# Optimization experiments

Measured on AMD Instinct MI355X. Metric: run time of the kernel, lower is better.

## Reference

```python
import jax, jax.numpy as jnp
import numpy as np

N = 50000
E = 800000
HID = 128
EIN = 2 * HID + 1  # h[row] ++ h[col] ++ edge_attr
NC = 3             # n_coords
DIM = 3            # spatial dim
NORM_FACTOR = 100.0
LN_EPS = 1e-5


def layernorm(x, g, b):
    m = jnp.mean(x, axis=-1, keepdims=True)
    v = jnp.mean(jnp.square(x - m), axis=-1, keepdims=True)
    return (x - m) * jax.lax.rsqrt(v + LN_EPS) * g + b


def setup_inputs() -> dict:
    key = jax.random.key(0)
    ks = jax.random.split(key, 12)
    h = jax.random.normal(ks[0], (N, HID), dtype=jnp.float32)
    coord = jax.random.normal(ks[1], (N, NC, DIM), dtype=jnp.float32)
    coord_diff = jax.random.normal(ks[2], (E, NC, DIM), dtype=jnp.float32)
    edge_attr = jax.random.normal(ks[3], (E, 1), dtype=jnp.float32)
    edge_mask = jnp.ones((E, 1), dtype=jnp.float32)
    node_mask = jnp.ones((N, 1, 1), dtype=jnp.float32)
    row = jax.random.randint(ks[4], (E,), 0, N, dtype=jnp.int32)
    col = jax.random.randint(ks[5], (E,), 0, N, dtype=jnp.int32)
    # MLP params (stored [in, out])
    def xavier(k, fi, fo, gain=1.0):
        lim = gain * np.sqrt(6.0 / (fi + fo))
        return jax.random.uniform(k, (fi, fo), dtype=jnp.float32, minval=-lim, maxval=lim)
    W1 = xavier(ks[6], EIN, HID)
    b1 = jnp.zeros((HID,), jnp.float32)
    g1 = jnp.ones((HID,), jnp.float32)
    be1 = jnp.zeros((HID,), jnp.float32)
    W2 = xavier(ks[7], HID, HID)
    b2 = jnp.zeros((HID,), jnp.float32)
    g2 = jnp.ones((HID,), jnp.float32)
    be2 = jnp.zeros((HID,), jnp.float32)
    W3 = xavier(ks[8], HID, NC * NC, gain=0.01)  # final layer, no bias
    return dict(h=h, coord=coord, coord_diff=coord_diff, edge_attr=edge_attr,
                edge_mask=edge_mask, node_mask=node_mask, row=row, col=col,
                W1=W1, b1=b1, g1=g1, be1=be1, W2=W2, b2=b2, g2=g2, be2=be2, W3=W3)


def reference(h, coord, coord_diff, edge_attr, edge_mask, node_mask, row, col,
              W1, b1, g1, be1, W2, b2, g2, be2, W3):
    # gather node feats into edge features: [E, 2*HID + 1]
    x = jnp.concatenate([h[row], h[col], edge_attr], axis=1)
    x = jax.nn.silu(layernorm(x @ W1 + b1, g1, be1))
    x = jax.nn.silu(layernorm(x @ W2 + b2, g2, be2))
    phi = (x @ W3).reshape(-1, NC, NC)               # [E, NC, NC]
    trans = jnp.einsum('ejk,ejl->elk', coord_diff, phi)  # [E, NC, DIM]
    trans = trans * edge_mask[:, None]               # [E,1,1] broadcast
    agg = jax.ops.segment_sum(trans, row, num_segments=coord.shape[0]) / NORM_FACTOR
    return (coord + agg) * node_mask
```

## Files before the change

### kernel.cpp

```cpp
#include <hip/hip_runtime.h>
#include <hip/hip_bf16.h>

#define NN 50000
#define EE 800000

typedef __attribute__((ext_vector_type(8))) short short8;
typedef __attribute__((ext_vector_type(4))) short short4v;
typedef __attribute__((ext_vector_type(4))) float f32x4;

__device__ __forceinline__ float bf2f(ushort u) {
  union { unsigned u; float f; } v; v.u = ((unsigned)u) << 16; return v.f;
}
__device__ __forceinline__ ushort f2bf(float f) {
  union { float f; unsigned u; } v; v.f = f;
  unsigned r = v.u + 0x7FFFu + ((v.u >> 16) & 1u);
  return (ushort)(r >> 16);
}

__global__ void prep_h_kernel(const float* __restrict__ h, ushort* __restrict__ hb) {
  int i = blockIdx.x * 256 + threadIdx.x;
  const float4* p = (const float4*)h;
  float4 a = p[2*i], b = p[2*i+1];
  short8 o;
  o[0]=f2bf(a.x); o[1]=f2bf(a.y); o[2]=f2bf(a.z); o[3]=f2bf(a.w);
  o[4]=f2bf(b.x); o[5]=f2bf(b.y); o[6]=f2bf(b.z); o[7]=f2bf(b.w);
  *(short8*)(hb + 8*i) = o;
}

__global__ void prep_w_kernel(const float* __restrict__ W1, const float* __restrict__ W2,
                              const float* __restrict__ W3,
                              ushort* __restrict__ W1t, ushort* __restrict__ W2t,
                              ushort* __restrict__ W3t) {
  int i = blockIdx.x * 256 + threadIdx.x;
  if (i < 32768) {
    int n = i >> 8, k = i & 255;
    W1t[i] = f2bf(W1[k*128 + n]);
  } else if (i < 49152) {
    int j = i - 32768, n = j >> 7, k = j & 127;
    W2t[j] = f2bf(W2[k*128 + n]);
  } else if (i < 51200) {
    int j = i - 49152, n = j >> 7, k = j & 127;
    W3t[j] = (n < 9) ? f2bf(W3[k*9 + n]) : (ushort)0;
  }
}

__device__ __forceinline__ void ln_silu(const ushort* smT, ushort* smX,
                                        float* smRedS, float* smRedQ,
                                        const float* __restrict__ g,
                                        const float* __restrict__ be,
                                        int lane, int w) {
  int e = lane, n0 = w * 32;
  float s = 0.f, q = 0.f;
  #pragma unroll
  for (int i = 0; i < 32; ++i) {
    float f = bf2f(smT[(n0 + i)*72 + e]);
    s += f; q += f*f;
  }
  smRedS[w*64 + e] = s; smRedQ[w*64 + e] = q;
  __syncthreads();
  s = smRedS[e] + smRedS[64+e] + smRedS[128+e] + smRedS[192+e];
  q = smRedQ[e] + smRedQ[64+e] + smRedQ[128+e] + smRedQ[192+e];
  float m  = s * (1.f/128.f);
  float rs = rsqrtf(q * (1.f/128.f) - m*m + 1e-5f);
  #pragma unroll
  for (int c = 0; c < 4; ++c) {
    short8 o;
    #pragma unroll
    for (int j = 0; j < 8; ++j) {
      int i = c*8 + j;
      float f = bf2f(smT[(n0 + i)*72 + e]);
      float v = (f - m) * rs * g[n0 + i] + be[n0 + i];
      v = v * (1.f / (1.f + __expf(-v)));
      o[j] = f2bf(v);
    }
    int bo = (e*256 + (n0 + c*8)*2) ^ ((e & 7) << 4);
    *(short8*)((char*)smX + bo) = o;
  }
}

template<bool USE_HB>
__global__ __launch_bounds__(256, 2)
void edge_kernel(const float* __restrict__ h, const ushort* __restrict__ hb,
                 const ushort* __restrict__ W1t, const ushort* __restrict__ W2t,
                 const ushort* __restrict__ W3t,
                 const float* __restrict__ W1,
                 const float* __restrict__ b1, const float* __restrict__ g1, const float* __restrict__ be1,
                 const float* __restrict__ b2, const float* __restrict__ g2, const float* __restrict__ be2,
                 const float* __restrict__ edge_attr, const float* __restrict__ edge_mask,
                 const float* __restrict__ coord_diff,
                 const int* __restrict__ row, const int* __restrict__ col,
                 float* __restrict__ agg) {
  __shared__ __align__(16) ushort smA[64*256];
  __shared__ __align__(16) ushort smT[128*72];
  __shared__ __align__(16) ushort smX[64*128];
  __shared__ float smCd[64*9];
  __shared__ float smPhi[64*12];
  __shared__ float smRedS[256];
  __shared__ float smRedQ[256];
  __shared__ float smEA[64];
  __shared__ float smEM[64];
  __shared__ int   smRow[64];

  const int tid  = threadIdx.x;
  const int lane = tid & 63;
  const int w    = tid >> 6;
  const int l15  = lane & 15;
  const int lh   = lane >> 4;
  const int wm   = w >> 1;
  const int wn   = w & 1;
  const int e0   = blockIdx.x * 64;

  {
    int e = tid >> 2, p = tid & 3;
    int re = row[e0 + e], ce = col[e0 + e];
    if (p == 0) { smEA[e] = edge_attr[e0+e]; smEM[e] = edge_mask[e0+e]; smRow[e] = re; }
    if (USE_HB) {
      const ushort* s = hb + (size_t)((p & 2) ? ce : re) * 128 + (p & 1) * 64;
      #pragma unroll
      for (int c = 0; c < 8; ++c) {
        short8 v = *(const short8*)(s + c*8);
        int bo = (e*512 + (p*8 + c)*16) ^ ((e & 7) << 4);
        *(short8*)((char*)smA + bo) = v;
      }
    } else {
      const float* s = h + (size_t)((p & 2) ? ce : re) * 128 + (p & 1) * 64;
      #pragma unroll
      for (int c = 0; c < 8; ++c) {
        float4 a = *(const float4*)(s + c*8);
        float4 b = *(const float4*)(s + c*8 + 4);
        short8 v;
        v[0]=f2bf(a.x); v[1]=f2bf(a.y); v[2]=f2bf(a.z); v[3]=f2bf(a.w);
        v[4]=f2bf(b.x); v[5]=f2bf(b.y); v[6]=f2bf(b.z); v[7]=f2bf(b.w);
        int bo = (e*512 + (p*8 + c)*16) ^ ((e & 7) << 4);
        *(short8*)((char*)smA + bo) = v;
      }
    }
  }
  if (tid < 144)
    *(float4*)(smCd + tid*4) = *(const float4*)(coord_diff + (size_t)e0*9 + tid*4);
  __syncthreads();

  f32x4 acc[2][4] = {};
  {
    const ushort* Wp[4];
    #pragma unroll
    for (int nf = 0; nf < 4; ++nf)
      Wp[nf] = W1t + (size_t)(wn*64 + nf*16 + l15) * 256 + lh*8;
    #pragma unroll
    for (int k0 = 0; k0 < 8; ++k0) {
      short8 b[4];
      #pragma unroll
      for (int nf = 0; nf < 4; ++nf) b[nf] = *(const short8*)(Wp[nf] + k0*32);
      #pragma unroll
      for (int mi = 0; mi < 2; ++mi) {
        int r = wm*32 + mi*16 + l15;
        int bo = (r*512 + k0*64 + lh*16) ^ ((r & 7) << 4);
        short8 a = *(const short8*)((char*)smA + bo);
        #pragma unroll
        for (int nf = 0; nf < 4; ++nf)
          acc[mi][nf] = __builtin_amdgcn_mfma_f32_16x16x32_bf16(a, b[nf], acc[mi][nf], 0, 0, 0);
      }
    }
  }
  {
    const float* w1last = W1 + 256*128;
    #pragma unroll
    for (int nf = 0; nf < 4; ++nf) {
      int n = wn*64 + nf*16 + l15;
      float bb = b1[n], wl = w1last[n];
      #pragma unroll
      for (int mi = 0; mi < 2; ++mi) {
        int r0 = wm*32 + mi*16 + lh*4;
        short4v o;
        #pragma unroll
        for (int j = 0; j < 4; ++j)
          o[j] = f2bf(acc[mi][nf][j] + bb + smEA[r0 + j] * wl);
        *(short4v*)(smT + n*72 + r0) = o;
      }
    }
  }
  __syncthreads();
  ln_silu(smT, smX, smRedS, smRedQ, g1, be1, lane, w);
  __syncthreads();

  f32x4 acc2[2][4] = {};
  {
    const ushort* Wp[4];
    #pragma unroll
    for (int nf = 0; nf < 4; ++nf)
      Wp[nf] = W2t + (size_t)(wn*64 + nf*16 + l15) * 128 + lh*8;
    #pragma unroll
    for (int k0 = 0; k0 < 4; ++k0) {
      short8 b[4];
      #pragma unroll
      for (int nf = 0; nf < 4; ++nf) b[nf] = *(const short8*)(Wp[nf] + k0*32);
      #pragma unroll
      for (int mi = 0; mi < 2; ++mi) {
        int r = wm*32 + mi*16 + l15;
        int bo = (r*256 + k0*64 + lh*16) ^ ((r & 7) << 4);
        short8 a = *(const short8*)((char*)smX + bo);
        #pragma unroll
        for (int nf = 0; nf < 4; ++nf)
          acc2[mi][nf] = __builtin_amdgcn_mfma_f32_16x16x32_bf16(a, b[nf], acc2[mi][nf], 0, 0, 0);
      }
    }
  }
  {
    #pragma unroll
    for (int nf = 0; nf < 4; ++nf) {
      int n = wn*64 + nf*16 + l15;
      float bb = b2[n];
      #pragma unroll
      for (int mi = 0; mi < 2; ++mi) {
        int r0 = wm*32 + mi*16 + lh*4;
        short4v o;
        #pragma unroll
        for (int j = 0; j < 4; ++j) o[j] = f2bf(acc2[mi][nf][j] + bb);
        *(short4v*)(smT + n*72 + r0) = o;
      }
    }
  }
  __syncthreads();
  ln_silu(smT, smX, smRedS, smRedQ, g2, be2, lane, w);
  __syncthreads();

  {
    f32x4 acc3 = {};
    const ushort* Wp = W3t + (size_t)l15*128 + lh*8;
    #pragma unroll
    for (int k0 = 0; k0 < 4; ++k0) {
      short8 b = *(const short8*)(Wp + k0*32);
      int r = w*16 + l15;
      int bo = (r*256 + k0*64 + lh*16) ^ ((r & 7) << 4);
      short8 a = *(const short8*)((char*)smX + bo);
      acc3 = __builtin_amdgcn_mfma_f32_16x16x32_bf16(a, b, acc3, 0, 0, 0);
    }
    if (l15 < 9) {
      #pragma unroll
      for (int j = 0; j < 4; ++j)
        smPhi[(w*16 + lh*4 + j)*12 + l15] = acc3[j];
    }
  }
  __syncthreads();

  {
    int e = tid >> 2, q = tid & 3;
    int re = smRow[e];
    float em = smEM[e];
    const float* cd = smCd + e*9;
    const float* ph = smPhi + e*12;
    for (int idx = q; idx < 9; idx += 4) {
      int l2 = idx / 3, k = idx - l2*3;
      float t = cd[k]*ph[l2] + cd[3+k]*ph[3+l2] + cd[6+k]*ph[6+l2];
      unsafeAtomicAdd(&agg[(size_t)re*9 + idx], t * em);
    }
  }
}

__global__ void finalize_kernel(const float* __restrict__ coord, const float* __restrict__ node_mask,
                                const float* __restrict__ agg, float* __restrict__ out) {
  int i = blockIdx.x * 256 + threadIdx.x;
  if (i < NN*9) {
    int n = i / 9;
    out[i] = (coord[i] + agg[i] * 0.01f) * node_mask[n];
  }
}

extern "C" void kernel_launch(void* const* d_in, const int* in_sizes, int n_in,
                              void* d_out, int out_size, void* d_ws, size_t ws_size,
                              hipStream_t stream) {
  const float* h          = (const float*)d_in[0];
  const float* coord      = (const float*)d_in[1];
  const float* coord_diff = (const float*)d_in[2];
  const float* edge_attr  = (const float*)d_in[3];
  const float* edge_mask  = (const float*)d_in[4];
  const float* node_mask  = (const float*)d_in[5];
  const int*   rowi       = (const int*)d_in[6];
  const int*   coli       = (const int*)d_in[7];
  const float* W1  = (const float*)d_in[8];
  const float* b1  = (const float*)d_in[9];
  const float* g1  = (const float*)d_in[10];
  const float* be1 = (const float*)d_in[11];
  const float* W2  = (const float*)d_in[12];
  const float* b2  = (const float*)d_in[13];
  const float* g2  = (const float*)d_in[14];
  const float* be2 = (const float*)d_in[15];
  const float* W3  = (const float*)d_in[16];

  char* ws = (char*)d_ws;
  float*  agg = (float*)ws;
  ushort* W1t = (ushort*)(ws + 1800064);
  ushort* W2t = (ushort*)(ws + 1865600);
  ushort* W3t = (ushort*)(ws + 1898368);
  ushort* hb  = (ushort*)(ws + 1902464);
  bool use_hb = ws_size >= (size_t)1902464 + 12800000;

  hipMemsetAsync(agg, 0, (size_t)NN*9*sizeof(float), stream);
  prep_w_kernel<<<200, 256, 0, stream>>>(W1, W2, W3, W1t, W2t, W3t);
  if (use_hb) {
    prep_h_kernel<<<NN*128/(8*256), 256, 0, stream>>>(h, hb);
    edge_kernel<true><<<EE/64, 256, 0, stream>>>(h, hb, W1t, W2t, W3t, W1,
        b1, g1, be1, b2, g2, be2, edge_attr, edge_mask, coord_diff, rowi, coli, agg);
  } else {
    edge_kernel<false><<<EE/64, 256, 0, stream>>>(h, hb, W1t, W2t, W3t, W1,
        b1, g1, be1, b2, g2, be2, edge_attr, edge_mask, coord_diff, rowi, coli, agg);
  }
  finalize_kernel<<<(NN*9 + 255)/256, 256, 0, stream>>>(coord, node_mask, agg, (float*)d_out);
}
```

Before: 601.9 us.

## Alias shared buffers, do LayerNorm in place, merge prep launches, raise occupancy

The MFMA outputs are now written straight into the swizzled row-major activation buffer. LayerNorm+SiLU then runs in place, with each thread caching its 32 values in registers, so the transposed staging buffer is gone. The gather buffer and activation buffer share one shared-memory region, which cuts LDS per block from about 75KB to 35KB, and launch bounds are raised to allow 4 blocks per CU. The weight/h bf16 conversion kernels and the agg memset are merged into one prep launch, and SiLU uses a hardware reciprocal. In exchange there are extra barriers, scalar 2-byte LDS stores that may bank-conflict, and higher register pressure under the tighter launch bound.

```diff
diff --git a/kernel.cpp b/kernel.cpp
--- a/kernel.cpp
+++ b/kernel.cpp
@@ -5,7 +5,6 @@
 #define EE 800000
 
 typedef __attribute__((ext_vector_type(8))) short short8;
-typedef __attribute__((ext_vector_type(4))) short short4v;
 typedef __attribute__((ext_vector_type(4))) float f32x4;
 
 __device__ __forceinline__ float bf2f(ushort u) {
@@ -17,46 +16,54 @@
   return (ushort)(r >> 16);
 }
 
-__global__ void prep_h_kernel(const float* __restrict__ h, ushort* __restrict__ hb) {
-  int i = blockIdx.x * 256 + threadIdx.x;
-  const float4* p = (const float4*)h;
-  float4 a = p[2*i], b = p[2*i+1];
-  short8 o;
-  o[0]=f2bf(a.x); o[1]=f2bf(a.y); o[2]=f2bf(a.z); o[3]=f2bf(a.w);
-  o[4]=f2bf(b.x); o[5]=f2bf(b.y); o[6]=f2bf(b.z); o[7]=f2bf(b.w);
-  *(short8*)(hb + 8*i) = o;
-}
-
-__global__ void prep_w_kernel(const float* __restrict__ W1, const float* __restrict__ W2,
-                              const float* __restrict__ W3,
-                              ushort* __restrict__ W1t, ushort* __restrict__ W2t,
-                              ushort* __restrict__ W3t) {
-  int i = blockIdx.x * 256 + threadIdx.x;
-  if (i < 32768) {
-    int n = i >> 8, k = i & 255;
-    W1t[i] = f2bf(W1[k*128 + n]);
-  } else if (i < 49152) {
-    int j = i - 32768, n = j >> 7, k = j & 127;
-    W2t[j] = f2bf(W2[k*128 + n]);
-  } else if (i < 51200) {
-    int j = i - 49152, n = j >> 7, k = j & 127;
-    W3t[j] = (n < 9) ? f2bf(W3[k*9 + n]) : (ushort)0;
-  }
-}
-
-__device__ __forceinline__ void ln_silu(const ushort* smT, ushort* smX,
-                                        float* smRedS, float* smRedQ,
-                                        const float* __restrict__ g,
-                                        const float* __restrict__ be,
-                                        int lane, int w) {
-  int e = lane, n0 = w * 32;
-  float s = 0.f, q = 0.f;
+__global__ void prep_kernel(const float* __restrict__ h, ushort* __restrict__ hb,
+                            const float* __restrict__ W1, const float* __restrict__ W2,
+                            const float* __restrict__ W3,
+                            ushort* __restrict__ W1t, ushort* __restrict__ W2t,
+                            ushort* __restrict__ W3t, float* __restrict__ agg) {
+  int b = blockIdx.x, tid = threadIdx.x;
+  if (b < 3125) {
+    int i = b * 256 + tid;
+    const float4* p = (const float4*)h;
+    float4 a = p[2*i], c = p[2*i+1];
+    short8 o;
+    o[0]=f2bf(a.x); o[1]=f2bf(a.y); o[2]=f2bf(a.z); o[3]=f2bf(a.w);
+    o[4]=f2bf(c.x); o[5]=f2bf(c.y); o[6]=f2bf(c.z); o[7]=f2bf(c.w);
+    *(short8*)(hb + 8*i) = o;
+  } else if (b < 3325) {
+    int i = (b - 3125) * 256 + tid;
+    if (i < 32768) {
+      int n = i >> 8, k = i & 255;
+      W1t[i] = f2bf(W1[k*128 + n]);
+    } else if (i < 49152) {
+      int j = i - 32768, n = j >> 7, k = j & 127;
+      W2t[j] = f2bf(W2[k*128 + n]);
+    } else if (i < 51200) {
+      int j = i - 49152, n = j >> 7, k = j & 127;
+      W3t[j] = (n < 9) ? f2bf(W3[k*9 + n]) : (ushort)0;
+    }
+  } else {
+    int i = (b - 3325) * 256 + tid;
+    if (i < NN*9) agg[i] = 0.f;
+  }
+}
+
+__device__ __forceinline__ void ln_silu_inplace(ushort* smX, float* smRedS, float* smRedQ,
+                                                const float* __restrict__ g,
+                                                const float* __restrict__ be, int tid) {
+  int e = tid & 63, w4 = tid >> 6, n0 = w4 * 32;
+  float v[32]; float s = 0.f, q = 0.f;
+  int bo[4];
   #pragma unroll
-  for (int i = 0; i < 32; ++i) {
-    float f = bf2f(smT[(n0 + i)*72 + e]);
-    s += f; q += f*f;
-  }
-  smRedS[w*64 + e] = s; smRedQ[w*64 + e] = q;
+  for (int c = 0; c < 4; ++c) {
+    bo[c] = (e*256 + (n0 + c*8)*2) ^ ((e & 7) << 4);
+    short8 x = *(const short8*)((char*)smX + bo[c]);
+    #pragma unroll
+    for (int j = 0; j < 8; ++j) {
+      float f = bf2f((ushort)x[j]); v[c*8+j] = f; s += f; q += f*f;
+    }
+  }
+  smRedS[w4*64 + e] = s; smRedQ[w4*64 + e] = q;
   __syncthreads();
   s = smRedS[e] + smRedS[64+e] + smRedS[128+e] + smRedS[192+e];
   q = smRedQ[e] + smRedQ[64+e] + smRedQ[128+e] + smRedQ[192+e];
@@ -67,19 +74,17 @@
     short8 o;
     #pragma unroll
     for (int j = 0; j < 8; ++j) {
-      int i = c*8 + j;
-      float f = bf2f(smT[(n0 + i)*72 + e]);
-      float v = (f - m) * rs * g[n0 + i] + be[n0 + i];
-      v = v * (1.f / (1.f + __expf(-v)));
-      o[j] = f2bf(v);
-    }
-    int bo = (e*256 + (n0 + c*8)*2) ^ ((e & 7) << 4);
-    *(short8*)((char*)smX + bo) = o;
-  }
+      float val = (v[c*8+j] - m) * rs * g[n0 + c*8 + j] + be[n0 + c*8 + j];
+      val = val * __builtin_amdgcn_rcpf(1.f + __expf(-val));
+      o[j] = f2bf(val);
+    }
+    *(short8*)((char*)smX + bo[c]) = o;
+  }
+  __syncthreads();
 }
 
 template<bool USE_HB>
-__global__ __launch_bounds__(256, 2)
+__global__ __launch_bounds__(256, 4)
 void edge_kernel(const float* __restrict__ h, const ushort* __restrict__ hb,
                  const ushort* __restrict__ W1t, const ushort* __restrict__ W2t,
                  const ushort* __restrict__ W3t,
@@ -90,16 +95,16 @@
                  const float* __restrict__ coord_diff,
                  const int* __restrict__ row, const int* __restrict__ col,
                  float* __restrict__ agg) {
-  __shared__ __align__(16) ushort smA[64*256];
-  __shared__ __align__(16) ushort smT[128*72];
-  __shared__ __align__(16) ushort smX[64*128];
-  __shared__ float smCd[64*9];
-  __shared__ float smPhi[64*12];
-  __shared__ float smRedS[256];
-  __shared__ float smRedQ[256];
-  __shared__ float smEA[64];
-  __shared__ float smEM[64];
-  __shared__ int   smRow[64];
+  __shared__ __align__(16) char smem[35840];
+  ushort* smA   = (ushort*)smem;
+  ushort* smX   = (ushort*)smem;
+  float*  smRedS = (float*)(smem + 16384);
+  float*  smRedQ = (float*)(smem + 17408);
+  float*  smPhi  = (float*)(smem + 18432);
+  float*  smCd   = (float*)(smem + 32768);
+  float*  smEA   = (float*)(smem + 35072);
+  float*  smEM   = (float*)(smem + 35328);
+  int*    smRow  = (int*)  (smem + 35584);
 
   const int tid  = threadIdx.x;
   const int lane = tid & 63;
@@ -127,10 +132,10 @@
       #pragma unroll
       for (int c = 0; c < 8; ++c) {
         float4 a = *(const float4*)(s + c*8);
-        float4 b = *(const float4*)(s + c*8 + 4);
+        float4 bq = *(const float4*)(s + c*8 + 4);
         short8 v;
         v[0]=f2bf(a.x); v[1]=f2bf(a.y); v[2]=f2bf(a.z); v[3]=f2bf(a.w);
-        v[4]=f2bf(b.x); v[5]=f2bf(b.y); v[6]=f2bf(b.z); v[7]=f2bf(b.w);
+        v[4]=f2bf(bq.x); v[5]=f2bf(bq.y); v[6]=f2bf(bq.z); v[7]=f2bf(bq.w);
         int bo = (e*512 + (p*8 + c)*16) ^ ((e & 7) << 4);
         *(short8*)((char*)smA + bo) = v;
       }
@@ -162,26 +167,36 @@
       }
     }
   }
+  __syncthreads();
+
   {
     const float* w1last = W1 + 256*128;
+    float bbv[4], wlv[4];
     #pragma unroll
     for (int nf = 0; nf < 4; ++nf) {
       int n = wn*64 + nf*16 + l15;
-      float bb = b1[n], wl = w1last[n];
-      #pragma unroll
-      for (int mi = 0; mi < 2; ++mi) {
-        int r0 = wm*32 + mi*16 + lh*4;
-        short4v o;
+      bbv[nf] = b1[n]; wlv[nf] = w1last[n];
+    }
+    #pragma unroll
+    for (int mi = 0; mi < 2; ++mi) {
+      int r0 = wm*32 + mi*16 + lh*4;
+      float ea[4];
+      #pragma unroll
+      for (int j = 0; j < 4; ++j) ea[j] = smEA[r0 + j];
+      #pragma unroll
+      for (int nf = 0; nf < 4; ++nf) {
+        int n = wn*64 + nf*16 + l15;
         #pragma unroll
-        for (int j = 0; j < 4; ++j)
-          o[j] = f2bf(acc[mi][nf][j] + bb + smEA[r0 + j] * wl);
-        *(short4v*)(smT + n*72 + r0) = o;
-      }
-    }
-  }
-  __syncthreads();
-  ln_silu(smT, smX, smRedS, smRedQ, g1, be1, lane, w);
-  __syncthreads();
+        for (int j = 0; j < 4; ++j) {
+          int r = r0 + j;
+          float val = acc[mi][nf][j] + bbv[nf] + ea[j] * wlv[nf];
+          *(ushort*)((char*)smX + ((r*256 + n*2) ^ ((r & 7) << 4))) = f2bf(val);
+        }
+      }
+    }
+  }
+  __syncthreads();
+  ln_silu_inplace(smX, smRedS, smRedQ, g1, be1, tid);
 
   f32x4 acc2[2][4] = {};
   {
@@ -205,24 +220,29 @@
       }
     }
   }
-  {
-    #pragma unroll
-    for (int nf = 0; nf < 4; ++nf) {
-      int n = wn*64 + nf*16 + l15;
-      float bb = b2[n];
-      #pragma unroll
-      for (int mi = 0; mi < 2; ++mi) {
-        int r0 = wm*32 + mi*16 + lh*4;
-        short4v o;
+  __syncthreads();
+
+  {
+    float bbv[4];
+    #pragma unroll
+    for (int nf = 0; nf < 4; ++nf) bbv[nf] = b2[wn*64 + nf*16 + l15];
+    #pragma unroll
+    for (int mi = 0; mi < 2; ++mi) {
+      int r0 = wm*32 + mi*16 + lh*4;
+      #pragma unroll
+      for (int nf = 0; nf < 4; ++nf) {
+        int n = wn*64 + nf*16 + l15;
         #pragma unroll
-        for (int j = 0; j < 4; ++j) o[j] = f2bf(acc2[mi][nf][j] + bb);
-        *(short4v*)(smT + n*72 + r0) = o;
-      }
-    }
-  }
-  __syncthreads();
-  ln_silu(smT, smX, smRedS, smRedQ, g2, be2, lane, w);
-  __syncthreads();
+        for (int j = 0; j < 4; ++j) {
+          int r = r0 + j;
+          float val = acc2[mi][nf][j] + bbv[nf];
+          *(ushort*)((char*)smX + ((r*256 + n*2) ^ ((r & 7) << 4))) = f2bf(val);
+        }
+      }
+    }
+  }
+  __syncthreads();
+  ln_silu_inplace(smX, smRedS, smRedQ, g2, be2, tid);
 
   {
     f32x4 acc3 = {};
@@ -244,12 +264,12 @@
   __syncthreads();
 
   {
-    int e = tid >> 2, q = tid & 3;
+    int e = tid >> 2, qd = tid & 3;
     int re = smRow[e];
     float em = smEM[e];
     const float* cd = smCd + e*9;
     const float* ph = smPhi + e*12;
-    for (int idx = q; idx < 9; idx += 4) {
+    for (int idx = qd; idx < 9; idx += 4) {
       int l2 = idx / 3, k = idx - l2*3;
       float t = cd[k]*ph[l2] + cd[3+k]*ph[3+l2] + cd[6+k]*ph[6+l2];
       unsafeAtomicAdd(&agg[(size_t)re*9 + idx], t * em);
@@ -295,13 +315,12 @@
   ushort* hb  = (ushort*)(ws + 1902464);
   bool use_hb = ws_size >= (size_t)1902464 + 12800000;
 
-  hipMemsetAsync(agg, 0, (size_t)NN*9*sizeof(float), stream);
-  prep_w_kernel<<<200, 256, 0, stream>>>(W1, W2, W3, W1t, W2t, W3t);
   if (use_hb) {
-    prep_h_kernel<<<NN*128/(8*256), 256, 0, stream>>>(h, hb);
+    prep_kernel<<<3325 + (NN*9 + 255)/256, 256, 0, stream>>>(h, hb, W1, W2, W3, W1t, W2t, W3t, agg);
     edge_kernel<true><<<EE/64, 256, 0, stream>>>(h, hb, W1t, W2t, W3t, W1,
         b1, g1, be1, b2, g2, be2, edge_attr, edge_mask, coord_diff, rowi, coli, agg);
   } else {
+    prep_kernel<<<3325 + (NN*9 + 255)/256, 256, 0, stream>>>(h, hb, W1, W2, W3, W1t, W2t, W3t, agg);
     edge_kernel<false><<<EE/64, 256, 0, stream>>>(h, hb, W1t, W2t, W3t, W1,
         b1, g1, be1, b2, g2, be2, edge_attr, edge_mask, coord_diff, rowi, coli, agg);
   }
```

Result: faster. 519.7 us (-13.7%).
